# Optimization experiments

Hardware: AMD Instinct MI355X
Metric: run time of the kernel (lower is better)

The kernel has to match this reference:

```python
import jax, jax.numpy as jnp
import numpy as np

EPS = 1.1920929e-07  # torch.finfo(float32).eps
TOP_K = 2
AUX_COEF = 0.01

def rmsnorm(x):
    return x * jax.lax.rsqrt(jnp.mean(x * x, axis=-1, keepdims=True) + EPS)

def setup_inputs() -> dict:
    key = jax.random.key(0)
    ks = jax.random.split(key, 8)
    B, T, C, H, E = 1, 2048, 1024, 2048, 8
    x = jax.random.normal(ks[0], (B, T, C), jnp.float32)
    gate_w = jax.random.normal(ks[1], (E, C), jnp.float32) * 0.02
    w1 = jax.random.normal(ks[2], (E, H, C), jnp.float32) * 0.02  # expert up-proj
    w2 = jax.random.normal(ks[3], (E, C, H), jnp.float32) * 0.02  # expert down-proj
    shared_gate_w = jax.random.normal(ks[4], (1, C), jnp.float32) * 0.02
    k_w = jax.random.normal(ks[5], (H, C), jnp.float32) * 0.02
    k_b = jax.random.normal(ks[6], (H,), jnp.float32) * 0.01
    v_w = jax.random.normal(ks[7], (C, H), jnp.float32) * 0.02
    v_b = jnp.zeros((C,), jnp.float32)
    return dict(x=x, gate_w=gate_w, w1=w1, w2=w2, shared_gate_w=shared_gate_w,
                k_w=k_w, k_b=k_b, v_w=v_w, v_b=v_b)

def reference(x, gate_w, w1, w2, shared_gate_w, k_w, k_b, v_w, v_b):
    B, T, C = x.shape
    xt = rmsnorm(x.reshape(-1, C))                     # [N,C]
    N = xt.shape[0]
    raw = xt @ gate_w.T                                # [N,E]
    scores = jax.nn.softmax(raw, axis=-1)
    topk_w, topk_idx = jax.lax.top_k(scores, TOP_K)    # [N,k]
    topk_w = topk_w / (jnp.sum(topk_w, axis=-1, keepdims=True) + 1e-6)
    E = scores.shape[-1]
    rows = jnp.arange(N)[:, None]
    onehot = jnp.zeros_like(scores).at[rows, topk_idx].set(1.0 / TOP_K)
    aux_loss = E * jnp.sum(jnp.mean(onehot, 0) * jnp.mean(scores, 0)) * AUX_COEF
    # dense gate matrix [N,E]: combine weight per (token, expert)
    g = jnp.zeros_like(scores).at[rows, topk_idx].add(topk_w)
    # grouped-GEMM expressed densely over experts (reference math identical)
    h = jnp.einsum('nc,ehc->neh', xt, w1)              # [N,E,H]
    h = jnp.square(jax.nn.relu(h)) * g[:, :, None]     # act + gate-combine weight
    out = jnp.einsum('neh,ech->nc', h, w2)             # [N,C]
    # shared expert: sigmoid gate * MLP (MLP re-norms its input)
    sg = jax.nn.sigmoid(xt @ shared_gate_w.T)          # [N,1]
    xs = rmsnorm(xt)
    kk = jnp.square(jax.nn.relu(xs @ k_w.T + k_b))     # [N,H]
    shared = kk @ v_w.T + v_b                          # [N,C]
    out = out + sg * shared
    return out.reshape(B, T, C), aux_loss
```

## Files before the change

kernel.cpp:

```cpp
#include <hip/hip_runtime.h>
#include <hip/hip_bf16.h>
#include <stdint.h>

typedef __bf16 bf16;
typedef bf16 bf16x8 __attribute__((ext_vector_type(8)));
typedef bf16 bf16x4 __attribute__((ext_vector_type(4)));
typedef float f32x4 __attribute__((ext_vector_type(4)));

constexpr int N = 2048;
constexpr int C = 1024;
constexpr int H = 2048;
constexpr int E = 8;
constexpr float EPS = 1.1920929e-07f;

constexpr int BM = 128, BN = 128, BK = 32;
constexpr int GT = 32;

constexpr int PREP_GATE = N / GT;
constexpr int PREP_RMS  = N;
constexpr int CVT1_F4   = (E * H * C + H * C) / 4;
constexpr int CVT1_BLK  = CVT1_F4 / 1024;
constexpr int PREP_TOTAL = PREP_GATE + PREP_RMS + CVT1_BLK;

constexpr int P1_UP    = (H / BN) * (N / BM) * E;
constexpr int P1_KP    = (N / BM) * (H / BN);
constexpr int CVT2_F4  = (E * C * H + C * H) / 4;
constexpr int CVT2_BLK = CVT2_F4 / 1024;
constexpr int P1_TOTAL = P1_UP + P1_KP + CVT2_BLK;

constexpr int P2_DOWN  = (C / BN) * (N / BM) * (E * 2);
constexpr int P2_VP    = (N / BM) * (C / BN) * 2;
constexpr int P2_TOTAL = P2_DOWN + P2_VP;

__device__ __forceinline__ void cvt_pair(const float* __restrict__ s1, bf16* __restrict__ d1,
                                         size_t n1, const float* __restrict__ s2,
                                         bf16* __restrict__ d2, int cbx) {
  size_t base = (size_t)cbx * 1024 + threadIdx.x;
  #pragma unroll
  for (int j = 0; j < 4; ++j) {
    size_t i = base + (size_t)j * 256;
    if (i < n1) {
      float4 v = ((const float4*)s1)[i];
      bf16x4 o = { (bf16)v.x, (bf16)v.y, (bf16)v.z, (bf16)v.w };
      ((bf16x4*)d1)[i] = o;
    } else {
      size_t k = i - n1;
      float4 v = ((const float4*)s2)[k];
      bf16x4 o = { (bf16)v.x, (bf16)v.y, (bf16)v.z, (bf16)v.w };
      ((bf16x4*)d2)[k] = o;
    }
  }
}

__global__ __launch_bounds__(256) void prep_kernel(
    const float* __restrict__ x, const float* __restrict__ gate_w,
    const float* __restrict__ sgw, const float* __restrict__ w1,
    const float* __restrict__ kw,
    bf16* __restrict__ xtb, float* __restrict__ rs2_arr,
    float* __restrict__ g, float* __restrict__ sgbuf,
    int* __restrict__ counts, int* __restrict__ lists,
    float* __restrict__ scoresums,
    bf16* __restrict__ w1b, bf16* __restrict__ kwb) {
  __shared__ float wsm[9][1024];
  __shared__ float s_scores[8];
  __shared__ int   s_cnt[8];
  __shared__ int   s_base[8];
  __shared__ int   s_e1[GT], s_p1[GT], s_e2[GT], s_p2[GT];
  const int bx = blockIdx.x;
  const int tid = threadIdx.x, lane = tid & 63, wave = tid >> 6;

  if (bx >= PREP_GATE + PREP_RMS) {
    cvt_pair(w1, w1b, (size_t)E * H * C / 4, kw, kwb, bx - PREP_GATE - PREP_RMS);
    return;
  }
  if (bx >= PREP_GATE) {
    int n = bx - PREP_GATE;
    float4 v = ((const float4*)(x + (size_t)n * C))[tid];
    float ss = v.x*v.x + v.y*v.y + v.z*v.z + v.w*v.w;
    #pragma unroll
    for (int off = 32; off > 0; off >>= 1) ss += __shfl_down(ss, off, 64);
    __shared__ float red[4];
    __shared__ float tot;
    if (lane == 0) red[wave] = ss;
    __syncthreads();
    if (tid == 0) tot = red[0] + red[1] + red[2] + red[3];
    __syncthreads();
    float sumsq = tot;
    float rs1 = rsqrtf(sumsq * (1.f / C) + EPS);
    bf16x4 o = { (bf16)(v.x*rs1), (bf16)(v.y*rs1), (bf16)(v.z*rs1), (bf16)(v.w*rs1) };
    ((bf16x4*)(xtb + (size_t)n * C))[tid] = o;
    if (tid == 0) {
      float m2 = sumsq * rs1 * rs1 * (1.f / C);
      rs2_arr[n] = rsqrtf(m2 + EPS);
    }
    return;
  }
  for (int i = tid; i < 9 * 1024; i += 256) {
    int e = i >> 10, c = i & 1023;
    wsm[e][c] = (e < 8) ? gate_w[i] : sgw[c];
  }
  if (tid < 8) { s_scores[tid] = 0.f; s_cnt[tid] = 0; }
  __syncthreads();

  const int tok0 = bx * GT + wave * (GT / 4);
  for (int tt = 0; tt < GT / 4; ++tt) {
    const int tok = tok0 + tt;
    const float* xr = x + (size_t)tok * C;
    float acc[10];
    #pragma unroll
    for (int e = 0; e < 10; e++) acc[e] = 0.f;
    #pragma unroll
    for (int k = 0; k < 16; ++k) {
      int c = k * 64 + lane;
      float xv = xr[c];
      #pragma unroll
      for (int e = 0; e < 9; e++) acc[e] = fmaf(xv, wsm[e][c], acc[e]);
      acc[9] = fmaf(xv, xv, acc[9]);
    }
    #pragma unroll
    for (int e = 0; e < 10; e++) {
      float v = acc[e];
      #pragma unroll
      for (int off = 32; off > 0; off >>= 1) v += __shfl_xor(v, off, 64);
      acc[e] = v;
    }
    if (lane == 0) {
      float rs1 = rsqrtf(acc[9] * (1.f / C) + EPS);
      float raw[9];
      #pragma unroll
      for (int e = 0; e < 9; e++) raw[e] = acc[e] * rs1;
      float m = raw[0];
      for (int e = 1; e < 8; e++) m = fmaxf(m, raw[e]);
      float sc[8], s = 0.f;
      for (int e = 0; e < 8; e++) { sc[e] = expf(raw[e] - m); s += sc[e]; }
      float inv = 1.f / s;
      for (int e = 0; e < 8; e++) sc[e] *= inv;
      int i1 = 0;
      for (int e = 1; e < 8; e++) if (sc[e] > sc[i1]) i1 = e;
      int i2 = -1;
      for (int e = 0; e < 8; e++) {
        if (e == i1) continue;
        if (i2 < 0 || sc[e] > sc[i2]) i2 = e;
      }
      float denom = sc[i1] + sc[i2] + 1e-6f;
      float* gr = g + (size_t)tok * E;
      #pragma unroll
      for (int e = 0; e < 8; e++) gr[e] = 0.f;
      gr[i1] = sc[i1] / denom;
      gr[i2] = sc[i2] / denom;
      sgbuf[tok] = 1.f / (1.f + expf(-raw[8]));
      for (int e = 0; e < 8; e++) atomicAdd(&s_scores[e], sc[e]);
      int lt = wave * (GT / 4) + tt;
      int p1 = atomicAdd(&s_cnt[i1], 1);
      int p2 = atomicAdd(&s_cnt[i2], 1);
      s_e1[lt] = i1; s_p1[lt] = p1;
      s_e2[lt] = i2; s_p2[lt] = p2;
    }
  }
  __syncthreads();
  if (tid < 8) {
    s_base[tid] = atomicAdd(&counts[tid], s_cnt[tid]);
    atomicAdd(&scoresums[tid], s_scores[tid]);
  }
  __syncthreads();
  if (tid < GT) {
    int tok = bx * GT + tid;
    int e1 = s_e1[tid], e2 = s_e2[tid];
    lists[e1 * N + s_base[e1] + s_p1[tid]] = (tok << 1);
    lists[e2 * N + s_base[e2] + s_p2[tid]] = (tok << 1) | 1;
  }
}

__device__ __forceinline__ void mfma_loop(
    const char* gA0, const char* gA1, const char* gB0, const char* gB1,
    char* As, char* Bs, int wave, int lane, int kIters,
    int mb, int nb, f32x4 acc[4][4]) {
  const int l0 = wave * 2048, l1 = l0 + 1024;
  const int arow = lane & 15;
  const int koff = (lane >> 4) * 16;
  for (int kt = 0; kt < kIters; ++kt) {
    __builtin_amdgcn_global_load_lds((__attribute__((address_space(1))) void*)gA0,
                                     (__attribute__((address_space(3))) void*)(As + l0), 16, 0, 0);
    __builtin_amdgcn_global_load_lds((__attribute__((address_space(1))) void*)gA1,
                                     (__attribute__((address_space(3))) void*)(As + l1), 16, 0, 0);
    __builtin_amdgcn_global_load_lds((__attribute__((address_space(1))) void*)gB0,
                                     (__attribute__((address_space(3))) void*)(Bs + l0), 16, 0, 0);
    __builtin_amdgcn_global_load_lds((__attribute__((address_space(1))) void*)gB1,
                                     (__attribute__((address_space(3))) void*)(Bs + l1), 16, 0, 0);
    gA0 += BK * 2; gA1 += BK * 2; gB0 += BK * 2; gB1 += BK * 2;
    __syncthreads();
    bf16x8 a[4], b[4];
    #pragma unroll
    for (int i = 0; i < 4; ++i) {
      a[i] = *(const bf16x8*)(As + (mb + i * 16 + arow) * 64 + koff);
      b[i] = *(const bf16x8*)(Bs + (nb + i * 16 + arow) * 64 + koff);
    }
    #pragma unroll
    for (int i = 0; i < 4; ++i)
      #pragma unroll
      for (int j = 0; j < 4; ++j)
        acc[i][j] = __builtin_amdgcn_mfma_f32_16x16x32_bf16(a[i], b[j], acc[i][j], 0, 0, 0);
    __syncthreads();
  }
}

#define GEMM_VARS                                                  \
  const int tid = threadIdx.x;                                     \
  const int lane = tid & 63, wave = tid >> 6;                      \
  const int sr0 = wave * 32 + (lane >> 2), sr1 = sr0 + 16;         \
  const int scb = (lane & 3) * 16;          \
  const int mb = (wave & 1) * 64, nb = (wave >> 1) * 64;           \
  const int col = lane & 15, quad = lane >> 4;                     \
  f32x4 acc[4][4] = {};

__device__ __forceinline__ void run_up(
    const bf16* __restrict__ xtb, const bf16* __restrict__ w1b,
    const float* __restrict__ g, const int* __restrict__ lists,
    const int* __restrict__ counts, bf16* __restrict__ hb,
    int e, int m0, int h0, char* As, char* Bs, int* toks) {
  const int cnt = counts[e];
  if (m0 >= cnt) return;
  GEMM_VARS
  if (tid < BM) toks[tid] = lists[e * N + min(m0 + tid, cnt - 1)];
  __syncthreads();
  const char* gA0 = (const char*)xtb + ((size_t)(toks[sr0] >> 1) * C) * 2 + scb;
  const char* gA1 = (const char*)xtb + ((size_t)(toks[sr1] >> 1) * C) * 2 + scb;
  const char* gB0 = (const char*)w1b + ((size_t)e * H * C + (size_t)(h0 + sr0) * C) * 2 + scb;
  const char* gB1 = (const char*)w1b + ((size_t)e * H * C + (size_t)(h0 + sr1) * C) * 2 + scb;
  mfma_loop(gA0, gA1, gB0, gB1, As, Bs, wave, lane, C / BK, mb, nb, acc);
  #pragma unroll
  for (int mi = 0; mi < 4; mi++) {
    #pragma unroll
    for (int r = 0; r < 4; r++) {
      int ml = mb + mi * 16 + quad * 4 + r;
      if (m0 + ml < cnt) {
        int packed = toks[ml];
        float gv = g[(size_t)(packed >> 1) * E + e];
        size_t base = (size_t)packed * H + h0 + nb;
        #pragma unroll
        for (int ni = 0; ni < 4; ni++) {
          float v = fmaxf(acc[mi][ni][r], 0.f);
          hb[base + ni * 16 + col] = (bf16)(v * v * gv);
        }
      }
    }
  }
}

__device__ __forceinline__ void run_kproj(
    const bf16* __restrict__ xtb, const bf16* __restrict__ kwb,
    const float* __restrict__ rs2, const float* __restrict__ k_b,
    bf16* __restrict__ kkb, int n0, int h0, char* As, char* Bs) {
  GEMM_VARS
  const char* gA0 = (const char*)xtb + ((size_t)(n0 + sr0) * C) * 2 + scb;
  const char* gA1 = (const char*)xtb + ((size_t)(n0 + sr1) * C) * 2 + scb;
  const char* gB0 = (const char*)kwb + ((size_t)(h0 + sr0) * C) * 2 + scb;
  const char* gB1 = (const char*)kwb + ((size_t)(h0 + sr1) * C) * 2 + scb;
  mfma_loop(gA0, gA1, gB0, gB1, As, Bs, wave, lane, C / BK, mb, nb, acc);
  #pragma unroll
  for (int mi = 0; mi < 4; mi++) {
    #pragma unroll
    for (int r = 0; r < 4; r++) {
      int n = n0 + mb + mi * 16 + quad * 4 + r;
      float rs = rs2[n];
      #pragma unroll
      for (int ni = 0; ni < 4; ni++) {
        int h = h0 + nb + ni * 16 + col;
        float v = fmaf(acc[mi][ni][r], rs, k_b[h]);
        v = fmaxf(v, 0.f);
        kkb[(size_t)n * H + h] = (bf16)(v * v);
      }
    }
  }
}

__device__ __forceinline__ void run_down(
    const bf16* __restrict__ hb, const bf16* __restrict__ w2b,
    const int* __restrict__ lists, const int* __restrict__ counts,
    float* __restrict__ out, int e, int ks, int m0, int c0,
    char* As, char* Bs, int* toks) {
  const int cnt = counts[e];
  if (m0 >= cnt) return;
  GEMM_VARS
  if (tid < BM) toks[tid] = lists[e * N + min(m0 + tid, cnt - 1)];
  __syncthreads();
  const size_t kofs = (size_t)ks * (H / 2) * 2;
  const char* gA0 = (const char*)hb + ((size_t)toks[sr0] * H) * 2 + kofs + scb;
  const char* gA1 = (const char*)hb + ((size_t)toks[sr1] * H) * 2 + kofs + scb;
  const char* gB0 = (const char*)w2b + ((size_t)e * C * H + (size_t)(c0 + sr0) * H) * 2 + kofs + scb;
  const char* gB1 = (const char*)w2b + ((size_t)e * C * H + (size_t)(c0 + sr1) * H) * 2 + kofs + scb;
  mfma_loop(gA0, gA1, gB0, gB1, As, Bs, wave, lane, (H / 2) / BK, mb, nb, acc);
  #pragma unroll
  for (int mi = 0; mi < 4; mi++) {
    #pragma unroll
    for (int r = 0; r < 4; r++) {
      int ml = mb + mi * 16 + quad * 4 + r;
      if (m0 + ml < cnt) {
        int tok = toks[ml] >> 1;
        float* orow = out + (size_t)tok * C + c0 + nb;
        #pragma unroll
        for (int ni = 0; ni < 4; ni++) atomicAdd(&orow[ni * 16 + col], acc[mi][ni][r]);
      }
    }
  }
}

__device__ __forceinline__ void run_vproj(
    const bf16* __restrict__ kkb, const bf16* __restrict__ vwb,
    const float* __restrict__ v_b, const float* __restrict__ sg,
    float* __restrict__ out, int n0, int c0, int ks, char* As, char* Bs) {
  GEMM_VARS
  const size_t kofs = (size_t)ks * (H / 2) * 2;
  const char* gA0 = (const char*)kkb + ((size_t)(n0 + sr0) * H) * 2 + kofs + scb;
  const char* gA1 = (const char*)kkb + ((size_t)(n0 + sr1) * H) * 2 + kofs + scb;
  const char* gB0 = (const char*)vwb + ((size_t)(c0 + sr0) * H) * 2 + kofs + scb;
  const char* gB1 = (const char*)vwb + ((size_t)(c0 + sr1) * H) * 2 + kofs + scb;
  mfma_loop(gA0, gA1, gB0, gB1, As, Bs, wave, lane, (H / 2) / BK, mb, nb, acc);
  #pragma unroll
  for (int mi = 0; mi < 4; mi++) {
    #pragma unroll
    for (int r = 0; r < 4; r++) {
      int n = n0 + mb + mi * 16 + quad * 4 + r;
      float sgv = sg[n];
      #pragma unroll
      for (int ni = 0; ni < 4; ni++) {
        int c = c0 + nb + ni * 16 + col;
        float add = sgv * acc[mi][ni][r];
        if (ks == 0) add += sgv * v_b[c];
        atomicAdd(&out[(size_t)n * C + c], add);
      }
    }
  }
}

__global__ __launch_bounds__(256) void phase1_kernel(
    const bf16* __restrict__ xtb, const bf16* __restrict__ w1b,
    const float* __restrict__ g, const int* __restrict__ lists,
    const int* __restrict__ counts, bf16* __restrict__ hb,
    const bf16* __restrict__ kwb, const float* __restrict__ rs2,
    const float* __restrict__ k_b, bf16* __restrict__ kkb,
    const float* __restrict__ w2, const float* __restrict__ vw,
    bf16* __restrict__ w2b, bf16* __restrict__ vwb) {
  __shared__ __align__(16) char As[BM * BK * 2];
  __shared__ __align__(16) char Bs[BN * BK * 2];
  __shared__ int toks[BM];
  const int bx = blockIdx.x;
  if (bx < P1_UP) {
    int e = bx >> 8, rem = bx & 255;
    int h0 = (rem & 15) * BN, m0 = (rem >> 4) * BM;
    run_up(xtb, w1b, g, lists, counts, hb, e, m0, h0, As, Bs, toks);
  } else if (bx < P1_UP + P1_KP) {
    int rem = bx - P1_UP;
    int n0 = (rem & 15) * BM, h0 = (rem >> 4) * BN;
    run_kproj(xtb, kwb, rs2, k_b, kkb, n0, h0, As, Bs);
  } else {
    cvt_pair(w2, w2b, (size_t)E * C * H / 4, vw, vwb, bx - P1_UP - P1_KP);
  }
}

__global__ __launch_bounds__(256) void phase2_kernel(
    const bf16* __restrict__ hb, const bf16* __restrict__ w2b,
    const int* __restrict__ lists, const int* __restrict__ counts,
    const bf16* __restrict__ kkb, const bf16* __restrict__ vwb,
    const float* __restrict__ v_b, const float* __restrict__ sg,
    float* __restrict__ out) {
  __shared__ __align__(16) char As[BM * BK * 2];
  __shared__ __align__(16) char Bs[BN * BK * 2];
  __shared__ int toks[BM];
  const int bx = blockIdx.x;
  if (bx < P2_DOWN) {
    int z = bx >> 7, rem = bx & 127;
    int e = z >> 1, ks = z & 1;
    int c0 = (rem & 7) * BN, m0 = (rem >> 3) * BM;
    run_down(hb, w2b, lists, counts, out, e, ks, m0, c0, As, Bs, toks);
  } else {
    int rem = bx - P2_DOWN;
    int ks = rem >> 7, r2 = rem & 127;
    int n0 = (r2 & 15) * BM, c0 = (r2 >> 4) * BN;
    run_vproj(kkb, vwb, v_b, sg, out, n0, c0, ks, As, Bs);
  }
}

__global__ void aux_kernel(const float* __restrict__ scoresums,
                           const int* __restrict__ counts,
                           float* __restrict__ out_aux) {
  if (threadIdx.x == 0) {
    float a = 0.f;
    for (int e = 0; e < 8; e++)
      a += (0.5f * (float)counts[e] * (1.f / N)) * (scoresums[e] * (1.f / N));
    out_aux[0] = 8.f * a * 0.01f;
  }
}

extern "C" void kernel_launch(void* const* d_in, const int* in_sizes, int n_in,
                              void* d_out, int out_size, void* d_ws, size_t ws_size,
                              hipStream_t stream) {
  (void)in_sizes; (void)n_in; (void)ws_size;
  const float* x   = (const float*)d_in[0];
  const float* gw  = (const float*)d_in[1];
  const float* w1  = (const float*)d_in[2];
  const float* w2  = (const float*)d_in[3];
  const float* sgw = (const float*)d_in[4];
  const float* k_w = (const float*)d_in[5];
  const float* k_b = (const float*)d_in[6];
  const float* v_w = (const float*)d_in[7];
  const float* v_b = (const float*)d_in[8];
  float* out = (float*)d_out;

  char* p = (char*)d_ws;
  auto alloc = [&](size_t bytes) { char* r = p; p += (bytes + 255) & ~255ull; return r; };
  bf16* xtb  = (bf16*)alloc((size_t)N * C * 2);
  bf16* w1b  = (bf16*)alloc((size_t)E * H * C * 2);
  bf16* w2b  = (bf16*)alloc((size_t)E * C * H * 2);
  bf16* kwb  = (bf16*)alloc((size_t)H * C * 2);
  bf16* vwb  = (bf16*)alloc((size_t)C * H * 2);
  bf16* hb   = (bf16*)alloc((size_t)2 * N * H * 2);
  bf16* kkb  = (bf16*)alloc((size_t)N * H * 2);
  float* rs2 = (float*)alloc((size_t)N * 4);
  float* g   = (float*)alloc((size_t)N * E * 4);
  float* sg  = (float*)alloc((size_t)N * 4);
  float* scoresums = (float*)alloc(256);
  int* counts = (int*)alloc(256);
  int* lists  = (int*)alloc((size_t)E * N * 4);

  hipMemsetAsync(d_out, 0, (size_t)out_size * sizeof(float), stream);
  hipMemsetAsync(scoresums, 0, 512, stream);
  prep_kernel<<<PREP_TOTAL, 256, 0, stream>>>(
      x, gw, sgw, w1, k_w, xtb, rs2, g, sg, counts, lists, scoresums, w1b, kwb);
  phase1_kernel<<<P1_TOTAL, 256, 0, stream>>>(
      xtb, w1b, g, lists, counts, hb, kwb, rs2, k_b, kkb, w2, v_w, w2b, vwb);
  phase2_kernel<<<P2_TOTAL, 256, 0, stream>>>(
      hb, w2b, lists, counts, kkb, vwb, v_b, sg, out);
  aux_kernel<<<1, 64, 0, stream>>>(scoresums, counts, out + (size_t)N * C);
}
```

Measured before the change: 326.5 us.

## Replace atomic output accumulation with partial buffers and a combine kernel

The down-projection and shared-expert value-projection GEMMs no longer atomically add into the output. Each split-K and top-k slot now writes its partial tile to a dedicated fp32 buffer, reusing the w1 bf16 workspace for the expert partials. A new elementwise combine kernel sums the six partials and applies the sigmoid gate and bias. This removes contended fp32 atomics, at the cost of extra global memory traffic for the partials and one more kernel launch.

```diff
diff --git a/kernel.cpp b/kernel.cpp
--- a/kernel.cpp
+++ b/kernel.cpp
@@ -31,6 +31,8 @@
 constexpr int P2_DOWN  = (C / BN) * (N / BM) * (E * 2);
 constexpr int P2_VP    = (N / BM) * (C / BN) * 2;
 constexpr int P2_TOTAL = P2_DOWN + P2_VP;
+
+constexpr int COMBINE_BLK = (N * C / 4) / 256;
 
 __device__ __forceinline__ void cvt_pair(const float* __restrict__ s1, bf16* __restrict__ d1,
                                          size_t n1, const float* __restrict__ s2,
@@ -277,7 +279,7 @@
 __device__ __forceinline__ void run_down(
     const bf16* __restrict__ hb, const bf16* __restrict__ w2b,
     const int* __restrict__ lists, const int* __restrict__ counts,
-    float* __restrict__ out, int e, int ks, int m0, int c0,
+    float* __restrict__ dp, int e, int ks, int m0, int c0,
     char* As, char* Bs, int* toks) {
   const int cnt = counts[e];
   if (m0 >= cnt) return;
@@ -296,10 +298,11 @@
     for (int r = 0; r < 4; r++) {
       int ml = mb + mi * 16 + quad * 4 + r;
       if (m0 + ml < cnt) {
-        int tok = toks[ml] >> 1;
-        float* orow = out + (size_t)tok * C + c0 + nb;
+        int packed = toks[ml];
+        int tok = packed >> 1, par = packed & 1;
+        float* orow = dp + (((size_t)(ks * 2 + par) * N + tok) * C) + c0 + nb;
         #pragma unroll
-        for (int ni = 0; ni < 4; ni++) atomicAdd(&orow[ni * 16 + col], acc[mi][ni][r]);
+        for (int ni = 0; ni < 4; ni++) orow[ni * 16 + col] = acc[mi][ni][r];
       }
     }
   }
@@ -307,8 +310,7 @@
 
 __device__ __forceinline__ void run_vproj(
     const bf16* __restrict__ kkb, const bf16* __restrict__ vwb,
-    const float* __restrict__ v_b, const float* __restrict__ sg,
-    float* __restrict__ out, int n0, int c0, int ks, char* As, char* Bs) {
+    float* __restrict__ vp, int n0, int c0, int ks, char* As, char* Bs) {
   GEMM_VARS
   const size_t kofs = (size_t)ks * (H / 2) * 2;
   const char* gA0 = (const char*)kkb + ((size_t)(n0 + sr0) * H) * 2 + kofs + scb;
@@ -321,14 +323,9 @@
     #pragma unroll
     for (int r = 0; r < 4; r++) {
       int n = n0 + mb + mi * 16 + quad * 4 + r;
-      float sgv = sg[n];
-      #pragma unroll
-      for (int ni = 0; ni < 4; ni++) {
-        int c = c0 + nb + ni * 16 + col;
-        float add = sgv * acc[mi][ni][r];
-        if (ks == 0) add += sgv * v_b[c];
-        atomicAdd(&out[(size_t)n * C + c], add);
-      }
+      float* orow = vp + ((size_t)ks * N + n) * C + c0 + nb;
+      #pragma unroll
+      for (int ni = 0; ni < 4; ni++) orow[ni * 16 + col] = acc[mi][ni][r];
     }
   }
 }
@@ -362,8 +359,7 @@
     const bf16* __restrict__ hb, const bf16* __restrict__ w2b,
     const int* __restrict__ lists, const int* __restrict__ counts,
     const bf16* __restrict__ kkb, const bf16* __restrict__ vwb,
-    const float* __restrict__ v_b, const float* __restrict__ sg,
-    float* __restrict__ out) {
+    float* __restrict__ dp, float* __restrict__ vp) {
   __shared__ __align__(16) char As[BM * BK * 2];
   __shared__ __align__(16) char Bs[BN * BK * 2];
   __shared__ int toks[BM];
@@ -372,13 +368,38 @@
     int z = bx >> 7, rem = bx & 127;
     int e = z >> 1, ks = z & 1;
     int c0 = (rem & 7) * BN, m0 = (rem >> 3) * BM;
-    run_down(hb, w2b, lists, counts, out, e, ks, m0, c0, As, Bs, toks);
+    run_down(hb, w2b, lists, counts, dp, e, ks, m0, c0, As, Bs, toks);
   } else {
     int rem = bx - P2_DOWN;
     int ks = rem >> 7, r2 = rem & 127;
     int n0 = (r2 & 15) * BM, c0 = (r2 >> 4) * BN;
-    run_vproj(kkb, vwb, v_b, sg, out, n0, c0, ks, As, Bs);
-  }
+    run_vproj(kkb, vwb, vp, n0, c0, ks, As, Bs);
+  }
+}
+
+__global__ __launch_bounds__(256) void combine_kernel(
+    const float* __restrict__ dp, const float* __restrict__ vp,
+    const float* __restrict__ v_b, const float* __restrict__ sg,
+    float* __restrict__ out) {
+  constexpr size_t NC = (size_t)N * C;
+  size_t i = (size_t)blockIdx.x * 256 + threadIdx.x;
+  size_t off = i * 4;
+  int n = (int)(off >> 10);
+  int c = (int)(off & 1023);
+  float4 a = ((const float4*)(dp))[i];
+  float4 b = ((const float4*)(dp + NC))[i];
+  float4 d2 = ((const float4*)(dp + 2 * NC))[i];
+  float4 d3 = ((const float4*)(dp + 3 * NC))[i];
+  float4 u = ((const float4*)(vp))[i];
+  float4 w = ((const float4*)(vp + NC))[i];
+  float4 bias = *(const float4*)(v_b + c);
+  float s = sg[n];
+  float4 o;
+  o.x = a.x + b.x + d2.x + d3.x + s * (u.x + w.x + bias.x);
+  o.y = a.y + b.y + d2.y + d3.y + s * (u.y + w.y + bias.y);
+  o.z = a.z + b.z + d2.z + d3.z + s * (u.z + w.z + bias.z);
+  o.w = a.w + b.w + d2.w + d3.w + s * (u.w + w.w + bias.w);
+  ((float4*)out)[i] = o;
 }
 
 __global__ void aux_kernel(const float* __restrict__ scoresums,
@@ -422,6 +443,8 @@
   float* scoresums = (float*)alloc(256);
   int* counts = (int*)alloc(256);
   int* lists  = (int*)alloc((size_t)E * N * 4);
+  float* vp   = (float*)alloc((size_t)2 * N * C * 4);
+  float* dp   = (float*)w1b;
 
   hipMemsetAsync(d_out, 0, (size_t)out_size * sizeof(float), stream);
   hipMemsetAsync(scoresums, 0, 512, stream);
@@ -430,6 +453,7 @@
   phase1_kernel<<<P1_TOTAL, 256, 0, stream>>>(
       xtb, w1b, g, lists, counts, hb, kwb, rs2, k_b, kkb, w2, v_w, w2b, vwb);
   phase2_kernel<<<P2_TOTAL, 256, 0, stream>>>(
-      hb, w2b, lists, counts, kkb, vwb, v_b, sg, out);
+      hb, w2b, lists, counts, kkb, vwb, dp, vp);
+  combine_kernel<<<COMBINE_BLK, 256, 0, stream>>>(dp, vp, v_b, sg, out);
   aux_kernel<<<1, 64, 0, stream>>>(scoresums, counts, out + (size_t)N * C);
 }
```

Measured after the change: 304.4 us. 6.7% less time.
